# Kernel optimization log

Hardware: AMD Instinct MI355X
Metric: run time of the kernel (lower is better)

Reference implementation:

```python
import jax, jax.numpy as jnp
import numpy as np

EPS = 1e-8  # torch F.cosine_similarity eps


def _cos_attn_masked(x, roi, h):
    """Replicates MultiHeadedAttention_2: per-head cosine similarity, relu,
    global top-k(4) column mask (torch advanced-indexing semantics), roi mask.
    x: (B,num,C), roi: (B,num,num). Returns (B,num,num,h)."""
    B, num, C = x.shape
    dk = C // h
    xh = x.reshape(B, num, h, dk)
    n = jnp.linalg.norm(xh, axis=-1)                       # (B,num,h)
    dots = jnp.einsum('bihd,bjhd->bijh', xh, xh)           # (B,i,j,h)
    denom = jnp.maximum(n[:, :, None, :] * n[:, None, :, :], EPS)
    a = jax.nn.relu(dots / denom)                          # (B,i,j,h)
    # torch: values, idces = topk(attn, 4, dim=2); atten_mask[:, :, idces, :] = 1
    # -> column j is unmasked iff j appears ANYWHERE in idces (global union).
    _, idx = jax.lax.top_k(jnp.moveaxis(a, 2, -1), 4)      # (B,i,h,4) over j
    vec = jnp.zeros((num,), a.dtype).at[idx.reshape(-1)].set(1.0)
    return a * roi[:, :, :, None] * vec[None, None, :, None]


def _gconv_relu(x, w, b):
    """Grouped 1x1 Conv1d + ReLU. x: (B,C,num), w: (g, co_g, ci_g), b: (co,)."""
    B, C, num = x.shape
    g, co_g, ci_g = w.shape
    xg = x.reshape(B, g, ci_g, num)
    y = jnp.einsum('goc,bgcn->bgon', w, xg).reshape(B, g * co_g, num)
    return jax.nn.relu(y + b[None, :, None])


def setup_inputs() -> dict:
    key = jax.random.key(0)
    ks = jax.random.split(key, 10)
    B, num = 4, 1024
    c_in, c_mid, c_out, group = 256, 256, 256, 4
    inp = {
        'input': jax.random.normal(ks[0], (B, num, c_in), jnp.float32),
        'masks_roi': jax.random.randint(ks[1], (B, num, num), 0, 2, jnp.int32),
        'score_mask': jax.random.randint(ks[2], (B, num), 0, 2, jnp.int32),
        'gt_feat': jax.random.normal(ks[3], (B, num, c_in), jnp.float32),
        'w1': jax.random.normal(ks[4], (group, c_mid // group, c_in // group), jnp.float32) * 0.05,
        'b1': jax.random.normal(ks[5], (c_mid,), jnp.float32) * 0.05,
        'w2': jax.random.normal(ks[6], (group, c_out // group, c_mid // group), jnp.float32) * 0.05,
        'b2': jax.random.normal(ks[7], (c_out,), jnp.float32) * 0.05,
        'gt_w': jax.random.normal(ks[8], (c_out, c_in), jnp.float32) * 0.05,
        'gt_b': jax.random.normal(ks[9], (c_out,), jnp.float32) * 0.05,
        # module init explicitly zeroes LayerNorm weight AND bias
        'ln_w': jnp.zeros((c_out,), jnp.float32),
        'ln_b': jnp.zeros((c_out,), jnp.float32),
        'multi_head': 4,
    }
    return inp


def reference(input, masks_roi, score_mask, gt_feat, w1, b1, w2, b2, gt_w, gt_b, ln_w, ln_b, multi_head):
    h = multi_head
    B, num, C = input.shape
    dt = input.dtype
    sm = score_mask.astype(dt)
    roi = masks_roi.astype(dt) * sm[:, None, :]
    f_mask = jax.vmap(jnp.diag)((sm == 0).astype(dt))      # (B,num,num)

    gts = jax.nn.relu(gt_feat @ gt_w.T + gt_b).reshape(B, -1, gt_w.shape[0])

    # --- stage 1 ---
    a1 = (_cos_attn_masked(input, roi, h) + f_mask[:, :, :, None]) / 4.0
    p1 = a1.transpose(0, 3, 2, 1)                          # (B,h,j,i)
    out1 = _gconv_relu(input.transpose(0, 2, 1), w1, b1)   # (B,mid,num)
    mid = out1.shape[1]
    o1m = jnp.einsum('bhcj,bhji->bhci', out1.reshape(B, h, mid // h, num), p1)
    out1 = out1 + o1m.reshape(B, mid, num)

    # --- stage 2 ---
    a2 = (_cos_attn_masked(out1.transpose(0, 2, 1), roi, h) + f_mask[:, :, :, None]) / 4.0
    p2 = a2.transpose(0, 3, 2, 1)
    out2 = _gconv_relu(out1, w2, b2)                       # (B,out,num)
    co = out2.shape[1]
    o2m = jnp.einsum('bhcj,bhji->bhci', out2.reshape(B, h, co // h, num), p2)
    y = o2m.reshape(B, co, num).transpose(0, 2, 1)         # (B,num,out)

    # LayerNorm(eps=1e-6) -- weight/bias zero-initialized per the module
    mu = y.mean(-1, keepdims=True)
    var = y.var(-1, keepdims=True)
    node_feat = (y - mu) / jnp.sqrt(var + 1e-6) * ln_w + ln_b

    out2 = out2 + node_feat.transpose(0, 2, 1)
    return out2.transpose(0, 2, 1), gts, node_feat


if __name__ == '__main__':
    o = reference(**setup_inputs())
    print([x.shape for x in o])
```

## Files before the change

### kernel.cpp

```cpp
#include <hip/hip_runtime.h>
#include <hip/hip_bf16.h>

#define B_    4
#define NUM   1024
#define CH    256
#define HEADS 4
#define DK    64
#define LDK   72
#define NJC   4

typedef __hip_bfloat16 bf;
typedef __attribute__((ext_vector_type(8))) short short8;
typedef __attribute__((ext_vector_type(4))) float f32x4;
typedef unsigned long long u64;
typedef unsigned u32;

#define SEG_ ((size_t)B_ * NUM * CH)

__device__ inline bf tobf(float v) { return __float2bfloat16(v); }

__device__ inline void stage_tile(const float* __restrict__ src, size_t row0,
                                  int col0, int rowstride, bf (*dst)[LDK], int tid) {
  int r = tid >> 4, c4 = (tid & 15) * 4;
  #pragma unroll
  for (int it = 0; it < 4; ++it) {
    int row = r + it * 16;
    const float4 v = *(const float4*)&src[(row0 + row) * (size_t)rowstride + col0 + c4];
    union { bf h4[4]; short4 s4; } u;
    u.h4[0] = tobf(v.x); u.h4[1] = tobf(v.y); u.h4[2] = tobf(v.z); u.h4[3] = tobf(v.w);
    *(short4*)&dst[row][c4] = u.s4;
  }
}

__device__ inline void load_afrag_bf(const bf* __restrict__ arow, int quad, short8 af[2]) {
  af[0] = *(const short8*)&arow[quad * 8];
  af[1] = *(const short8*)&arow[32 + quad * 8];
}

__device__ inline u32 umax(u32 a, u32 b) { return a > b ? a : b; }
__device__ inline u32 umin(u32 a, u32 b) { return a < b ? a : b; }

__device__ inline void sort4(u32& k0, u32& k1, u32& k2, u32& k3) {
  u32 h;
  h = umax(k0, k1); k1 = umin(k0, k1); k0 = h;
  h = umax(k2, k3); k3 = umin(k2, k3); k2 = h;
  h = umax(k0, k2); k2 = umin(k0, k2); k0 = h;
  h = umax(k1, k3); k3 = umin(k1, k3); k1 = h;
  h = umax(k1, k2); k2 = umin(k1, k2); k1 = h;
}

__device__ inline void merge4(u32 t[4], u32 o0, u32 o1, u32 o2, u32 o3) {
  u32 m0 = umax(t[0], o3), m1 = umax(t[1], o2);
  u32 m2 = umax(t[2], o1), m3 = umax(t[3], o0);
  u32 h;
  h = umax(m0, m2); m2 = umin(m0, m2); m0 = h;
  h = umax(m1, m3); m3 = umin(m1, m3); m1 = h;
  h = umax(m0, m1); m1 = umin(m0, m1); m0 = h;
  h = umax(m2, m3); m3 = umin(m2, m3); m2 = h;
  t[0] = m0; t[1] = m1; t[2] = m2; t[3] = m3;
}

__device__ inline void conv_body(
    char* SM, int m0, int g, int tid,
    const float* __restrict__ x, const float* __restrict__ parts,
    const float* __restrict__ w,
    const float* __restrict__ bias, const int* __restrict__ smask,
    float seedbase, float* __restrict__ out, float* __restrict__ out2,
    float* __restrict__ rn, bf* __restrict__ xbf) {
  float (*Xs)[65] = (float(*)[65])SM;
  float (*Wsm)[65] = (float(*)[65])(SM + 16640);
  const int tx = tid & 15, ty = tid >> 4;
  #pragma unroll
  for (int l = 0; l < 16; ++l) {
    int idx = tid + l * 256; int r = idx >> 6, c = idx & 63;
    size_t gi = (size_t)(m0 + r) * CH + g * DK + c;
    float v = x[gi];
    if (parts)
      v += parts[gi] + parts[SEG_ + gi] + parts[2 * SEG_ + gi] + parts[3 * SEG_ + gi];
    Xs[r][c] = v;
    Wsm[r][c] = w[g * DK * DK + r * DK + c];
  }
  __syncthreads();
  {
    int r = tid >> 4, c4 = (tid & 15) * 4;
    #pragma unroll
    for (int it = 0; it < 4; ++it) {
      int row = r + it * 16;
      union { bf h4[4]; short4 s4; } u;
      u.h4[0] = tobf(Xs[row][c4]);     u.h4[1] = tobf(Xs[row][c4 + 1]);
      u.h4[2] = tobf(Xs[row][c4 + 2]); u.h4[3] = tobf(Xs[row][c4 + 3]);
      *(short4*)&xbf[(size_t)(m0 + row) * CH + g * DK + c4] = u.s4;
    }
  }
  {
    int wv = tid >> 6, lane = tid & 63;
    int row = wv * 16 + (lane >> 2), part = lane & 3;
    float s = 0.f;
    #pragma unroll
    for (int k = 0; k < 16; ++k) {
      float v = Xs[row][part * 16 + k];
      s += v * v;
    }
    s += __shfl_xor(s, 1, 64);
    s += __shfl_xor(s, 2, 64);
    if (part == 0)
      rn[(size_t)(m0 + row) * HEADS + g] = 1.0f / fmaxf(sqrtf(s), 1e-4f);
  }
  float acc[4][4] = {};
  #pragma unroll 8
  for (int k = 0; k < DK; ++k) {
    float av[4], bv[4];
    #pragma unroll
    for (int i = 0; i < 4; ++i) av[i] = Xs[ty * 4 + i][k];
    #pragma unroll
    for (int j = 0; j < 4; ++j) bv[j] = Wsm[tx * 4 + j][k];
    #pragma unroll
    for (int i = 0; i < 4; ++i)
      #pragma unroll
      for (int j = 0; j < 4; ++j) acc[i][j] += av[i] * bv[j];
  }
  #pragma unroll
  for (int i = 0; i < 4; ++i) {
    int row = m0 + ty * 4 + i;
    float seed = seedbase + ((smask[row] == 0) ? 0.25f : 0.f);
    #pragma unroll
    for (int j = 0; j < 4; ++j) {
      int o = g * DK + tx * 4 + j;
      size_t idx = (size_t)row * CH + o;
      float v = fmaxf(acc[i][j] + bias[o], 0.f);
      out[idx] = v;
      out2[idx] = v * seed;
    }
  }
}

__device__ inline void gts_body(
    char* SM, int m0, int n0, int tid,
    const float* __restrict__ gf, const float* __restrict__ gw,
    const float* __restrict__ gb, float* __restrict__ out) {
  bf (*As)[LDK] = (bf(*)[LDK])SM;
  bf (*Bs)[LDK] = (bf(*)[LDK])(SM + 9216);
  const int lane = tid & 63, w = tid >> 6;
  const int m = lane & 15, quad = lane >> 4;
  f32x4 acc[4] = {{0.f,0.f,0.f,0.f},{0.f,0.f,0.f,0.f},{0.f,0.f,0.f,0.f},{0.f,0.f,0.f,0.f}};
  for (int k0 = 0; k0 < 256; k0 += 64) {
    __syncthreads();
    stage_tile(gf, m0, k0, 256, As, tid);
    stage_tile(gw, n0, k0, 256, Bs, tid);
    __syncthreads();
    #pragma unroll
    for (int kb = 0; kb < 2; ++kb) {
      short8 a = *(const short8*)&As[w * 16 + m][kb * 32 + quad * 8];
      #pragma unroll
      for (int nt = 0; nt < 4; ++nt) {
        short8 bb = *(const short8*)&Bs[nt * 16 + m][kb * 32 + quad * 8];
        acc[nt] = __builtin_amdgcn_mfma_f32_16x16x32_bf16(a, bb, acc[nt], 0, 0, 0);
      }
    }
  }
  #pragma unroll
  for (int nt = 0; nt < 4; ++nt)
    #pragma unroll
    for (int r = 0; r < 4; ++r) {
      int row = m0 + w * 16 + quad * 4 + r, col = n0 + nt * 16 + m;
      out[(size_t)row * 256 + col] = fmaxf(acc[nt][r] + gb[col], 0.f);
    }
}

__device__ inline void pack_body(int blkrow, int tid, const int* __restrict__ mroi,
                                 const int* __restrict__ smask, u64* __restrict__ pk,
                                 float* __restrict__ v1, float* __restrict__ v2) {
  if (blkrow < 4) {
    int i = blkrow * 256 + tid;
    v1[i] = 0.f; v2[i] = 0.f;
  }
  int row = blkrow * 4 + (tid >> 6);
  int lane = tid & 63;
  int b = row >> 10;
  const int* mr = &mroi[(size_t)row * NUM];
  const int* sm = &smask[b * NUM];
  #pragma unroll
  for (int wd = 0; wd < 16; ++wd) {
    int j = wd * 64 + lane;
    u64 word = __ballot((mr[j] != 0) && (sm[j] != 0));
    if (lane == 0) pk[(size_t)row * 16 + wd] = word;
  }
}

__global__ __launch_bounds__(256) void head_kernel(
    const float* __restrict__ x, const float* __restrict__ w1,
    const float* __restrict__ b1, const int* __restrict__ smask,
    float* __restrict__ X1, float* __restrict__ F1, float* __restrict__ rn,
    bf* __restrict__ xbf,
    const float* __restrict__ gf, const float* __restrict__ gw,
    const float* __restrict__ gb, float* __restrict__ gts_out,
    const int* __restrict__ mroi, u64* __restrict__ pk,
    float* __restrict__ v1, float* __restrict__ v2) {
  __shared__ __align__(16) char SM[33280];
  const int tid = threadIdx.x;
  if (blockIdx.y < 4) {
    conv_body(SM, blockIdx.x * 64, blockIdx.y, tid, x, nullptr, w1, b1, smask,
              1.0f, X1, F1, rn, xbf);
  } else if (blockIdx.y < 8) {
    gts_body(SM, blockIdx.x * 64, (blockIdx.y - 4) * 64, tid, gf, gw, gb, gts_out);
  } else {
    pack_body((blockIdx.y - 8) * 64 + blockIdx.x, tid, mroi, smask, pk, v1, v2);
  }
}

__global__ __launch_bounds__(256) void conv_kernel(
    const float* __restrict__ x, const float* __restrict__ parts,
    const float* __restrict__ w,
    const float* __restrict__ bias, const int* __restrict__ smask,
    float seedbase, float* __restrict__ out, float* __restrict__ out2,
    float* __restrict__ rn, bf* __restrict__ xbf) {
  __shared__ __align__(16) char SM[33280];
  conv_body(SM, blockIdx.x * 64, blockIdx.y, threadIdx.x, x, parts, w, bias, smask,
            seedbase, out, out2, rn, xbf);
}

__global__ __launch_bounds__(256) void score_topk_kernel(
    const bf* __restrict__ xbf, const float* __restrict__ rn,
    const u64* __restrict__ pk, bf* __restrict__ wsout,
    u32* __restrict__ candK) {
  __shared__ __align__(16) bf Xj[2][64][LDK];
  const int b = blockIdx.z, h = blockIdx.y;
  const int it = blockIdx.x >> 2, jc = blockIdx.x & 3;
  const int i0 = it * 64;
  const int tid = threadIdx.x, lane = tid & 63, w = tid >> 6;
  const int m = lane & 15, quad = lane >> 4;
  const int srow = tid >> 3, schunk = tid & 7;

  short8 afrag[2];
  load_afrag_bf(&xbf[((size_t)b * NUM + i0 + w * 16 + m) * CH + h * DK], quad, afrag);

  u32 keys[4][4] = {};

  const int row0 = i0 + w * 16 + quad * 4;
  bf* wp[4];
  const u64* pkp[4];
  #pragma unroll
  for (int r = 0; r < 4; ++r) {
    wp[r]  = wsout + ((size_t)(b * HEADS + h) * NUM + row0 + r) * NUM + jc * 256 + m;
    pkp[r] = pk + ((size_t)b * NUM + row0 + r) * 16 + jc * 4;
  }
  const float* rnp = rn + ((size_t)b * NUM + jc * 256 + m) * HEADS + h;

  auto sload = [&](int jt, short8& n0, short8& n1) {
    size_t base = (size_t)b * NUM + jc * 256 + jt * 64;
    n0 = *(const short8*)&xbf[(base + srow) * CH + h * DK + schunk * 8];
    n1 = *(const short8*)&xbf[(base + srow + 32) * CH + h * DK + schunk * 8];
  };
  auto swrite = [&](int buf, short8 n0, short8 n1) {
    *(short8*)&Xj[buf][srow][schunk * 8] = n0;
    *(short8*)&Xj[buf][srow + 32][schunk * 8] = n1;
  };

  {
    short8 n0, n1;
    sload(0, n0, n1);
    swrite(0, n0, n1);
  }
  __syncthreads();

  #pragma unroll
  for (int jt = 0; jt < 4; ++jt) {
    const int cur = jt & 1;
    short8 n0, n1;
    if (jt < 3) sload(jt + 1, n0, n1);
    u64 wrm[4];
    float rnj4[4];
    #pragma unroll
    for (int r = 0; r < 4; ++r)
      wrm[r] = pkp[r][jt] >> m;
    #pragma unroll
    for (int nt = 0; nt < 4; ++nt)
      rnj4[nt] = rnp[(jt * 64 + nt * 16) * HEADS];

    f32x4 acc[4];
    #pragma unroll
    for (int nt = 0; nt < 4; ++nt) {
      acc[nt] = (f32x4){0.f, 0.f, 0.f, 0.f};
      #pragma unroll
      for (int kb = 0; kb < 2; ++kb) {
        short8 bb = *(const short8*)&Xj[cur][nt * 16 + m][kb * 32 + quad * 8];
        acc[nt] = __builtin_amdgcn_mfma_f32_16x16x32_bf16(afrag[kb], bb, acc[nt], 0, 0, 0);
      }
    }
    const u32 jinv0 = 1023u - (u32)(jc * 256 + jt * 64 + m);
    #pragma unroll
    for (int r = 0; r < 4; ++r) {
      float kv0 = fmaxf(acc[0][r] * rnj4[0], 0.f);
      float kv1 = fmaxf(acc[1][r] * rnj4[1], 0.f);
      float kv2 = fmaxf(acc[2][r] * rnj4[2], 0.f);
      float kv3 = fmaxf(acc[3][r] * rnj4[3], 0.f);
      u32 k0 = (__float_as_uint(kv0) & 0xFFFFFC00u) | jinv0;
      u32 k1 = (__float_as_uint(kv1) & 0xFFFFFC00u) | (jinv0 - 16u);
      u32 k2 = (__float_as_uint(kv2) & 0xFFFFFC00u) | (jinv0 - 32u);
      u32 k3 = (__float_as_uint(kv3) & 0xFFFFFC00u) | (jinv0 - 48u);
      sort4(k0, k1, k2, k3);
      merge4(keys[r], k0, k1, k2, k3);
      wp[r][jt * 64 +  0] = tobf((wrm[r] &        1ull) ? kv0 : 0.f);
      wp[r][jt * 64 + 16] = tobf((wrm[r] >> 16 &  1ull) ? kv1 : 0.f);
      wp[r][jt * 64 + 32] = tobf((wrm[r] >> 32 &  1ull) ? kv2 : 0.f);
      wp[r][jt * 64 + 48] = tobf((wrm[r] >> 48 &  1ull) ? kv3 : 0.f);
    }
    if (jt < 3) swrite(cur ^ 1, n0, n1);
    __syncthreads();
  }

  #pragma unroll
  for (int st = 1; st < 16; st <<= 1) {
    #pragma unroll
    for (int r = 0; r < 4; ++r) {
      u32 o0 = (u32)__shfl_xor((int)keys[r][0], st, 64);
      u32 o1 = (u32)__shfl_xor((int)keys[r][1], st, 64);
      u32 o2 = (u32)__shfl_xor((int)keys[r][2], st, 64);
      u32 o3 = (u32)__shfl_xor((int)keys[r][3], st, 64);
      merge4(keys[r], o0, o1, o2, o3);
    }
  }
  if (m == 0) {
    #pragma unroll
    for (int r = 0; r < 4; ++r) {
      int rl = w * 16 + quad * 4 + r;
      u32* dst = &candK[(size_t)((((b * HEADS + h) * 16 + it) * NJC + jc) * 64 + rl) * 4];
      #pragma unroll
      for (int q = 0; q < 4; ++q) dst[q] = keys[r][q];
    }
  }
}

__global__ __launch_bounds__(256) void topk_merge_kernel(
    const u32* __restrict__ candK, float* __restrict__ vec) {
  int t = blockIdx.x * 256 + threadIdx.x;
  int bhit = t >> 6, rl = t & 63;
  u32 best[4] = {};
  #pragma unroll
  for (int jc = 0; jc < NJC; ++jc) {
    const u32* c = &candK[(size_t)((bhit * NJC + jc) * 64 + rl) * 4];
    merge4(best, c[0], c[1], c[2], c[3]);
  }
  #pragma unroll
  for (int q = 0; q < 4; ++q)
    vec[1023u - (best[q] & 0x3FFu)] = 1.0f;
}

__global__ __launch_bounds__(256) void pv_kernel(
    const bf* __restrict__ wsin, const float* __restrict__ conv,
    const float* __restrict__ rn, const float* __restrict__ vec,
    float* __restrict__ outp) {
  __shared__ __align__(16) bf Cv[2][64][LDK];
  const int b = blockIdx.z, h = blockIdx.y;
  const int it = blockIdx.x >> 2, jc = blockIdx.x & 3;
  const int i0 = it * 64, jbase = jc * 256;
  const int tid = threadIdx.x, lane = tid & 63, w = tid >> 6;
  const int m = lane & 15, quad = lane >> 4;
  const int jr = tid >> 4, c4 = tid & 15;

  float rni4[4];
  #pragma unroll
  for (int r = 0; r < 4; ++r)
    rni4[r] = 0.25f * rn[((size_t)b * NUM + i0 + w * 16 + quad * 4 + r) * HEADS + h];

  const size_t wsrow = ((size_t)(b * HEADS + h) * NUM + i0 + w * 16 + m) * NUM + jbase;

  f32x4 om[4] = {{0.f,0.f,0.f,0.f},{0.f,0.f,0.f,0.f},{0.f,0.f,0.f,0.f},{0.f,0.f,0.f,0.f}};

  float4 pre[4]; float psc[4];
  auto issue = [&](int jt) {
    #pragma unroll
    for (int itt = 0; itt < 4; ++itt) {
      int j = jbase + jt * 64 + jr + itt * 16;
      psc[itt] = vec[j];
      pre[itt] = *(const float4*)&conv[((size_t)b * NUM + j) * CH + h * DK + c4 * 4];
    }
  };
  auto lwrite = [&](int buf) {
    #pragma unroll
    for (int itt = 0; itt < 4; ++itt) {
      int j = jr + itt * 16;
      Cv[buf][c4 * 4 + 0][j] = tobf(pre[itt].x * psc[itt]);
      Cv[buf][c4 * 4 + 1][j] = tobf(pre[itt].y * psc[itt]);
      Cv[buf][c4 * 4 + 2][j] = tobf(pre[itt].z * psc[itt]);
      Cv[buf][c4 * 4 + 3][j] = tobf(pre[itt].w * psc[itt]);
    }
  };

  issue(0); lwrite(0);
  short8 a0 = *(const short8*)&wsin[wsrow + quad * 8];
  short8 a1 = *(const short8*)&wsin[wsrow + 32 + quad * 8];

  for (int jt = 0; jt < 4; ++jt) {
    const int cur = jt & 1;
    short8 na0, na1;
    if (jt < 3) {
      issue(jt + 1);
      na0 = *(const short8*)&wsin[wsrow + (jt + 1) * 64 + quad * 8];
      na1 = *(const short8*)&wsin[wsrow + (jt + 1) * 64 + 32 + quad * 8];
    }
    __syncthreads();
    #pragma unroll
    for (int ct = 0; ct < 4; ++ct)
      om[ct] = __builtin_amdgcn_mfma_f32_16x16x32_bf16(
          a0, *(const short8*)&Cv[cur][ct * 16 + m][quad * 8], om[ct], 0, 0, 0);
    #pragma unroll
    for (int ct = 0; ct < 4; ++ct)
      om[ct] = __builtin_amdgcn_mfma_f32_16x16x32_bf16(
          a1, *(const short8*)&Cv[cur][ct * 16 + m][32 + quad * 8], om[ct], 0, 0, 0);
    if (jt < 3) { lwrite(cur ^ 1); a0 = na0; a1 = na1; }
  }

  const size_t ob = (size_t)(jc * B_ + b) * NUM;
  #pragma unroll
  for (int ct = 0; ct < 4; ++ct)
    #pragma unroll
    for (int r = 0; r < 4; ++r) {
      size_t idx = (ob + i0 + w * 16 + quad * 4 + r) * CH + h * DK + ct * 16 + m;
      outp[idx] = om[ct][r] * rni4[r];
    }
}

__global__ __launch_bounds__(256) void final_kernel(
    float* __restrict__ ybnf, float* __restrict__ out0,
    const float* __restrict__ lnw, const float* __restrict__ lnb,
    const float* __restrict__ parts) {
  __shared__ float r1[4];
  __shared__ float r2[4];
  int bn = blockIdx.x;
  int c = threadIdx.x;
  size_t idx = (size_t)bn * CH + c;
  float y = ybnf[idx] + parts[idx] + parts[SEG_ + idx]
          + parts[2 * SEG_ + idx] + parts[3 * SEG_ + idx];
  float x2v = out0[idx];
  float s = y;
  #pragma unroll
  for (int off = 32; off; off >>= 1) s += __shfl_down(s, off, 64);
  int wave = c >> 6, lane = c & 63;
  if (lane == 0) r1[wave] = s;
  __syncthreads();
  float mu = (r1[0] + r1[1] + r1[2] + r1[3]) * (1.f / 256.f);
  float d = y - mu;
  float s2 = d * d;
  #pragma unroll
  for (int off = 32; off; off >>= 1) s2 += __shfl_down(s2, off, 64);
  if (lane == 0) r2[wave] = s2;
  __syncthreads();
  float var = (r2[0] + r2[1] + r2[2] + r2[3]) * (1.f / 256.f);
  float nf = d * rsqrtf(var + 1e-6f) * lnw[c] + lnb[c];
  ybnf[idx] = nf;
  out0[idx] = x2v + nf;
}

extern "C" void kernel_launch(void* const* d_in, const int* in_sizes, int n_in,
                              void* d_out, int out_size, void* d_ws, size_t ws_size,
                              hipStream_t stream) {
  const float* input = (const float*)d_in[0];
  const int* mroi = (const int*)d_in[1];
  const int* smask = (const int*)d_in[2];
  const float* gt_feat = (const float*)d_in[3];
  const float* w1 = (const float*)d_in[4];
  const float* b1 = (const float*)d_in[5];
  const float* w2 = (const float*)d_in[6];
  const float* b2 = (const float*)d_in[7];
  const float* gt_w = (const float*)d_in[8];
  const float* gt_b = (const float*)d_in[9];
  const float* lnw = (const float*)d_in[10];
  const float* lnb = (const float*)d_in[11];

  const size_t SEG = SEG_;
  float* out0 = (float*)d_out;
  float* gts = out0 + SEG;
  float* nfreg = out0 + 2 * SEG;

  float* F1 = (float*)d_ws;
  float* RN = F1 + SEG;
  float* VEC1 = RN + (size_t)B_ * NUM * HEADS;
  float* VEC2 = VEC1 + NUM;
  u64* PK = (u64*)(VEC2 + NUM);
  bf* XBF = (bf*)(PK + (size_t)B_ * NUM * 16);
  bf* WSC = XBF + SEG;
  float* P = (float*)(WSC + (size_t)B_ * HEADS * NUM * NUM);
  u32* candK = (u32*)P;

  float* X1 = nfreg;
  float* X2 = out0;
  float* Yb = nfreg;

  head_kernel<<<dim3(64, 24), 256, 0, stream>>>(
      input, w1, b1, smask, X1, F1, RN, XBF,
      gt_feat, gt_w, gt_b, gts, mroi, PK, VEC1, VEC2);

  score_topk_kernel<<<dim3(16 * NJC, HEADS, B_), 256, 0, stream>>>(
      XBF, RN, PK, WSC, candK);
  topk_merge_kernel<<<64, 256, 0, stream>>>(candK, VEC1);
  pv_kernel<<<dim3(16 * NJC, HEADS, B_), 256, 0, stream>>>(WSC, X1, RN, VEC1, P);

  conv_kernel<<<dim3(64, 4), 256, 0, stream>>>(F1, P, w2, b2, smask, 0.0f, X2, Yb, RN, XBF);
  score_topk_kernel<<<dim3(16 * NJC, HEADS, B_), 256, 0, stream>>>(
      XBF, RN, PK, WSC, candK);
  topk_merge_kernel<<<64, 256, 0, stream>>>(candK, VEC2);
  pv_kernel<<<dim3(16 * NJC, HEADS, B_), 256, 0, stream>>>(WSC, X2, RN, VEC2, P);

  final_kernel<<<4096, 256, 0, stream>>>(Yb, X2, lnw, lnb, P);
}
```

Measured before the change: 199.4 us.

## Split score_topk j-tiles across two wave groups with 512-thread blocks

The score/top-k kernel now runs 512 threads per block. Two groups of four waves each handle half of the four j-tiles, so each wave does two tiles instead of four. All four Xj tiles are staged into shared memory once up front, which removes the per-tile double-buffer syncs. The two groups' partial top-4 keys are merged through a small shared exchange buffer. This adds parallelism and latency hiding per block, at the cost of more LDS per block and an extra barrier and merge step.

```diff
diff --git a/kernel.cpp b/kernel.cpp
--- a/kernel.cpp
+++ b/kernel.cpp
@@ -219,60 +219,53 @@
             seedbase, out, out2, rn, xbf);
 }
 
-__global__ __launch_bounds__(256) void score_topk_kernel(
+__global__ __launch_bounds__(512, 6) void score_topk_kernel(
     const bf* __restrict__ xbf, const float* __restrict__ rn,
     const u64* __restrict__ pk, bf* __restrict__ wsout,
     u32* __restrict__ candK) {
-  __shared__ __align__(16) bf Xj[2][64][LDK];
+  __shared__ __align__(16) bf Xj[4][64][LDK];
+  __shared__ u32 cexch[64][4];
   const int b = blockIdx.z, h = blockIdx.y;
   const int it = blockIdx.x >> 2, jc = blockIdx.x & 3;
   const int i0 = it * 64;
-  const int tid = threadIdx.x, lane = tid & 63, w = tid >> 6;
+  const int tid = threadIdx.x, lane = tid & 63, wv = tid >> 6;
   const int m = lane & 15, quad = lane >> 4;
+  const int g2 = wv >> 2, rw = wv & 3;
   const int srow = tid >> 3, schunk = tid & 7;
 
+  {
+    short8 st0, st1, st2, st3;
+    const bf* sb = &xbf[((size_t)b * NUM + jc * 256 + srow) * CH + h * DK + schunk * 8];
+    st0 = *(const short8*)&sb[0 * 64 * CH];
+    st1 = *(const short8*)&sb[1 * 64 * CH];
+    st2 = *(const short8*)&sb[2 * 64 * CH];
+    st3 = *(const short8*)&sb[3 * 64 * CH];
+    *(short8*)&Xj[0][srow][schunk * 8] = st0;
+    *(short8*)&Xj[1][srow][schunk * 8] = st1;
+    *(short8*)&Xj[2][srow][schunk * 8] = st2;
+    *(short8*)&Xj[3][srow][schunk * 8] = st3;
+  }
+
   short8 afrag[2];
-  load_afrag_bf(&xbf[((size_t)b * NUM + i0 + w * 16 + m) * CH + h * DK], quad, afrag);
+  load_afrag_bf(&xbf[((size_t)b * NUM + i0 + rw * 16 + m) * CH + h * DK], quad, afrag);
 
   u32 keys[4][4] = {};
 
-  const int row0 = i0 + w * 16 + quad * 4;
-  bf* wp[4];
-  const u64* pkp[4];
-  #pragma unroll
-  for (int r = 0; r < 4; ++r) {
-    wp[r]  = wsout + ((size_t)(b * HEADS + h) * NUM + row0 + r) * NUM + jc * 256 + m;
-    pkp[r] = pk + ((size_t)b * NUM + row0 + r) * 16 + jc * 4;
-  }
+  const int row0 = i0 + rw * 16 + quad * 4;
+  bf* wpb = wsout + ((size_t)(b * HEADS + h) * NUM + row0) * NUM + jc * 256 + m;
+  const u64* pkb = pk + ((size_t)b * NUM + row0) * 16 + jc * 4;
   const float* rnp = rn + ((size_t)b * NUM + jc * 256 + m) * HEADS + h;
 
-  auto sload = [&](int jt, short8& n0, short8& n1) {
-    size_t base = (size_t)b * NUM + jc * 256 + jt * 64;
-    n0 = *(const short8*)&xbf[(base + srow) * CH + h * DK + schunk * 8];
-    n1 = *(const short8*)&xbf[(base + srow + 32) * CH + h * DK + schunk * 8];
-  };
-  auto swrite = [&](int buf, short8 n0, short8 n1) {
-    *(short8*)&Xj[buf][srow][schunk * 8] = n0;
-    *(short8*)&Xj[buf][srow + 32][schunk * 8] = n1;
-  };
-
-  {
-    short8 n0, n1;
-    sload(0, n0, n1);
-    swrite(0, n0, n1);
-  }
   __syncthreads();
 
   #pragma unroll
-  for (int jt = 0; jt < 4; ++jt) {
-    const int cur = jt & 1;
-    short8 n0, n1;
-    if (jt < 3) sload(jt + 1, n0, n1);
+  for (int tt = 0; tt < 2; ++tt) {
+    const int jt = g2 * 2 + tt;
     u64 wrm[4];
     float rnj4[4];
     #pragma unroll
     for (int r = 0; r < 4; ++r)
-      wrm[r] = pkp[r][jt] >> m;
+      wrm[r] = pkb[r * 16 + jt] >> m;
     #pragma unroll
     for (int nt = 0; nt < 4; ++nt)
       rnj4[nt] = rnp[(jt * 64 + nt * 16) * HEADS];
@@ -283,7 +276,7 @@
       acc[nt] = (f32x4){0.f, 0.f, 0.f, 0.f};
       #pragma unroll
       for (int kb = 0; kb < 2; ++kb) {
-        short8 bb = *(const short8*)&Xj[cur][nt * 16 + m][kb * 32 + quad * 8];
+        short8 bb = *(const short8*)&Xj[jt][nt * 16 + m][kb * 32 + quad * 8];
         acc[nt] = __builtin_amdgcn_mfma_f32_16x16x32_bf16(afrag[kb], bb, acc[nt], 0, 0, 0);
       }
     }
@@ -300,13 +293,18 @@
       u32 k3 = (__float_as_uint(kv3) & 0xFFFFFC00u) | (jinv0 - 48u);
       sort4(k0, k1, k2, k3);
       merge4(keys[r], k0, k1, k2, k3);
-      wp[r][jt * 64 +  0] = tobf((wrm[r] &        1ull) ? kv0 : 0.f);
-      wp[r][jt * 64 + 16] = tobf((wrm[r] >> 16 &  1ull) ? kv1 : 0.f);
-      wp[r][jt * 64 + 32] = tobf((wrm[r] >> 32 &  1ull) ? kv2 : 0.f);
-      wp[r][jt * 64 + 48] = tobf((wrm[r] >> 48 &  1ull) ? kv3 : 0.f);
-    }
-    if (jt < 3) swrite(cur ^ 1, n0, n1);
-    __syncthreads();
+      if (tt == 0) {
+        wpb[r * NUM + g2 * 128 +  0] = tobf((wrm[r] &       1ull) ? kv0 : 0.f);
+        wpb[r * NUM + g2 * 128 + 16] = tobf((wrm[r] >> 16 & 1ull) ? kv1 : 0.f);
+        wpb[r * NUM + g2 * 128 + 32] = tobf((wrm[r] >> 32 & 1ull) ? kv2 : 0.f);
+        wpb[r * NUM + g2 * 128 + 48] = tobf((wrm[r] >> 48 & 1ull) ? kv3 : 0.f);
+      } else {
+        wpb[r * NUM + g2 * 128 + 64 +  0] = tobf((wrm[r] &       1ull) ? kv0 : 0.f);
+        wpb[r * NUM + g2 * 128 + 64 + 16] = tobf((wrm[r] >> 16 & 1ull) ? kv1 : 0.f);
+        wpb[r * NUM + g2 * 128 + 64 + 32] = tobf((wrm[r] >> 32 & 1ull) ? kv2 : 0.f);
+        wpb[r * NUM + g2 * 128 + 64 + 48] = tobf((wrm[r] >> 48 & 1ull) ? kv3 : 0.f);
+      }
+    }
   }
 
   #pragma unroll
@@ -320,10 +318,20 @@
       merge4(keys[r], o0, o1, o2, o3);
     }
   }
-  if (m == 0) {
+  if (g2 == 1 && m == 0) {
     #pragma unroll
     for (int r = 0; r < 4; ++r) {
-      int rl = w * 16 + quad * 4 + r;
+      int rl = rw * 16 + quad * 4 + r;
+      #pragma unroll
+      for (int q = 0; q < 4; ++q) cexch[rl][q] = keys[r][q];
+    }
+  }
+  __syncthreads();
+  if (g2 == 0 && m == 0) {
+    #pragma unroll
+    for (int r = 0; r < 4; ++r) {
+      int rl = rw * 16 + quad * 4 + r;
+      merge4(keys[r], cexch[rl][0], cexch[rl][1], cexch[rl][2], cexch[rl][3]);
       u32* dst = &candK[(size_t)((((b * HEADS + h) * 16 + it) * NJC + jc) * 64 + rl) * 4];
       #pragma unroll
       for (int q = 0; q < 4; ++q) dst[q] = keys[r][q];
@@ -491,13 +499,13 @@
       input, w1, b1, smask, X1, F1, RN, XBF,
       gt_feat, gt_w, gt_b, gts, mroi, PK, VEC1, VEC2);
 
-  score_topk_kernel<<<dim3(16 * NJC, HEADS, B_), 256, 0, stream>>>(
+  score_topk_kernel<<<dim3(16 * NJC, HEADS, B_), 512, 0, stream>>>(
       XBF, RN, PK, WSC, candK);
   topk_merge_kernel<<<64, 256, 0, stream>>>(candK, VEC1);
   pv_kernel<<<dim3(16 * NJC, HEADS, B_), 256, 0, stream>>>(WSC, X1, RN, VEC1, P);
 
   conv_kernel<<<dim3(64, 4), 256, 0, stream>>>(F1, P, w2, b2, smask, 0.0f, X2, Yb, RN, XBF);
-  score_topk_kernel<<<dim3(16 * NJC, HEADS, B_), 256, 0, stream>>>(
+  score_topk_kernel<<<dim3(16 * NJC, HEADS, B_), 512, 0, stream>>>(
       XBF, RN, PK, WSC, candK);
   topk_merge_kernel<<<64, 256, 0, stream>>>(candK, VEC2);
   pv_kernel<<<dim3(16 * NJC, HEADS, B_), 256, 0, stream>>>(WSC, X2, RN, VEC2, P);
```

After: 197.4 us. Within noise of the previous version (-1.0%).

## Fuse top-k merge into score kernel using 1024-thread blocks and LDS exchange

Applied to the files above, without the earlier changes.

The score/top-k kernel now runs one 1024-thread block per (b,h,row-tile), with four wave groups each covering a 256-column chunk. Partial top-4 candidates are merged through shared memory and written straight into the column mask. This removes the separate topk_merge launch and the global candidate round-trip, twice per forward. In exchange the grid shrinks from 1024 to 256 blocks, shared memory per block grows, and the launch-bounds hint of 4 blocks per SM may not be reachable, which could reduce occupancy.

```diff
diff --git a/kernel.cpp b/kernel.cpp
--- a/kernel.cpp
+++ b/kernel.cpp
@@ -219,41 +219,29 @@
             seedbase, out, out2, rn, xbf);
 }
 
-__global__ __launch_bounds__(256) void score_topk_kernel(
+__global__ __launch_bounds__(1024, 4) void score_topk_kernel(
     const bf* __restrict__ xbf, const float* __restrict__ rn,
     const u64* __restrict__ pk, bf* __restrict__ wsout,
-    u32* __restrict__ candK) {
-  __shared__ __align__(16) bf Xj[2][64][LDK];
-  const int b = blockIdx.z, h = blockIdx.y;
-  const int it = blockIdx.x >> 2, jc = blockIdx.x & 3;
+    float* __restrict__ vec) {
+  __shared__ __align__(16) bf Xj[2][4][64][LDK];
+  __shared__ u32 cexch[3][64][4];
+  const int b = blockIdx.z, h = blockIdx.y, it = blockIdx.x;
   const int i0 = it * 64;
-  const int tid = threadIdx.x, lane = tid & 63, w = tid >> 6;
+  const int tid = threadIdx.x, lane = tid & 63, wv = tid >> 6;
   const int m = lane & 15, quad = lane >> 4;
-  const int srow = tid >> 3, schunk = tid & 7;
-
-  short8 afrag[2];
-  load_afrag_bf(&xbf[((size_t)b * NUM + i0 + w * 16 + m) * CH + h * DK], quad, afrag);
-
-  u32 keys[4][4] = {};
-
-  const int row0 = i0 + w * 16 + quad * 4;
-  bf* wp[4];
-  const u64* pkp[4];
-  #pragma unroll
-  for (int r = 0; r < 4; ++r) {
-    wp[r]  = wsout + ((size_t)(b * HEADS + h) * NUM + row0 + r) * NUM + jc * 256 + m;
-    pkp[r] = pk + ((size_t)b * NUM + row0 + r) * 16 + jc * 4;
-  }
-  const float* rnp = rn + ((size_t)b * NUM + jc * 256 + m) * HEADS + h;
-
-  auto sload = [&](int jt, short8& n0, short8& n1) {
-    size_t base = (size_t)b * NUM + jc * 256 + jt * 64;
-    n0 = *(const short8*)&xbf[(base + srow) * CH + h * DK + schunk * 8];
-    n1 = *(const short8*)&xbf[(base + srow + 32) * CH + h * DK + schunk * 8];
+  const int g4 = wv >> 2, rw = wv & 3;
+  const int slot = tid & 511, srow = slot >> 3, schunk = slot & 7;
+  const int tpair = tid >> 9;
+
+  auto sload = [&](int k, short8& n0, short8& n1) {
+    size_t base = (size_t)b * NUM;
+    int t0 = (tpair * 2 + 0) * 4 + k, t1 = (tpair * 2 + 1) * 4 + k;
+    n0 = *(const short8*)&xbf[(base + t0 * 64 + srow) * CH + h * DK + schunk * 8];
+    n1 = *(const short8*)&xbf[(base + t1 * 64 + srow) * CH + h * DK + schunk * 8];
   };
   auto swrite = [&](int buf, short8 n0, short8 n1) {
-    *(short8*)&Xj[buf][srow][schunk * 8] = n0;
-    *(short8*)&Xj[buf][srow + 32][schunk * 8] = n1;
+    *(short8*)&Xj[buf][tpair * 2 + 0][srow][schunk * 8] = n0;
+    *(short8*)&Xj[buf][tpair * 2 + 1][srow][schunk * 8] = n1;
   };
 
   {
@@ -261,21 +249,34 @@
     sload(0, n0, n1);
     swrite(0, n0, n1);
   }
+
+  short8 afrag[2];
+  load_afrag_bf(&xbf[((size_t)b * NUM + i0 + rw * 16 + m) * CH + h * DK], quad, afrag);
+
+  u32 keys[4][4] = {};
+
+  const int row0 = i0 + rw * 16 + quad * 4;
+  bf* wpb = wsout + ((size_t)(b * HEADS + h) * NUM + row0) * NUM + m;
+  const u64* pkb = pk + ((size_t)b * NUM + row0) * 16;
+  const float* rnp = rn + ((size_t)b * NUM + m) * HEADS + h;
+
   __syncthreads();
 
   #pragma unroll
-  for (int jt = 0; jt < 4; ++jt) {
-    const int cur = jt & 1;
+  for (int k = 0; k < 4; ++k) {
+    const int cur = k & 1;
+    const int jt = g4 * 4 + k;
+    const int j0 = jt * 64;
     short8 n0, n1;
-    if (jt < 3) sload(jt + 1, n0, n1);
+    if (k < 3) sload(k + 1, n0, n1);
     u64 wrm[4];
     float rnj4[4];
     #pragma unroll
     for (int r = 0; r < 4; ++r)
-      wrm[r] = pkp[r][jt] >> m;
+      wrm[r] = pkb[r * 16 + jt] >> m;
     #pragma unroll
     for (int nt = 0; nt < 4; ++nt)
-      rnj4[nt] = rnp[(jt * 64 + nt * 16) * HEADS];
+      rnj4[nt] = rnp[(j0 + nt * 16) * HEADS];
 
     f32x4 acc[4];
     #pragma unroll
@@ -283,11 +284,11 @@
       acc[nt] = (f32x4){0.f, 0.f, 0.f, 0.f};
       #pragma unroll
       for (int kb = 0; kb < 2; ++kb) {
-        short8 bb = *(const short8*)&Xj[cur][nt * 16 + m][kb * 32 + quad * 8];
+        short8 bb = *(const short8*)&Xj[cur][g4][nt * 16 + m][kb * 32 + quad * 8];
         acc[nt] = __builtin_amdgcn_mfma_f32_16x16x32_bf16(afrag[kb], bb, acc[nt], 0, 0, 0);
       }
     }
-    const u32 jinv0 = 1023u - (u32)(jc * 256 + jt * 64 + m);
+    const u32 jinv0 = 1023u - (u32)(j0 + m);
     #pragma unroll
     for (int r = 0; r < 4; ++r) {
       float kv0 = fmaxf(acc[0][r] * rnj4[0], 0.f);
@@ -300,12 +301,12 @@
       u32 k3 = (__float_as_uint(kv3) & 0xFFFFFC00u) | (jinv0 - 48u);
       sort4(k0, k1, k2, k3);
       merge4(keys[r], k0, k1, k2, k3);
-      wp[r][jt * 64 +  0] = tobf((wrm[r] &        1ull) ? kv0 : 0.f);
-      wp[r][jt * 64 + 16] = tobf((wrm[r] >> 16 &  1ull) ? kv1 : 0.f);
-      wp[r][jt * 64 + 32] = tobf((wrm[r] >> 32 &  1ull) ? kv2 : 0.f);
-      wp[r][jt * 64 + 48] = tobf((wrm[r] >> 48 &  1ull) ? kv3 : 0.f);
-    }
-    if (jt < 3) swrite(cur ^ 1, n0, n1);
+      wpb[r * NUM + j0 +  0] = tobf((wrm[r] &        1ull) ? kv0 : 0.f);
+      wpb[r * NUM + j0 + 16] = tobf((wrm[r] >> 16 &  1ull) ? kv1 : 0.f);
+      wpb[r * NUM + j0 + 32] = tobf((wrm[r] >> 32 &  1ull) ? kv2 : 0.f);
+      wpb[r * NUM + j0 + 48] = tobf((wrm[r] >> 48 &  1ull) ? kv3 : 0.f);
+    }
+    if (k < 3) swrite(cur ^ 1, n0, n1);
     __syncthreads();
   }
 
@@ -320,30 +321,27 @@
       merge4(keys[r], o0, o1, o2, o3);
     }
   }
-  if (m == 0) {
+  if (g4 != 0 && m == 0) {
     #pragma unroll
     for (int r = 0; r < 4; ++r) {
-      int rl = w * 16 + quad * 4 + r;
-      u32* dst = &candK[(size_t)((((b * HEADS + h) * 16 + it) * NJC + jc) * 64 + rl) * 4];
+      int rl = rw * 16 + quad * 4 + r;
       #pragma unroll
-      for (int q = 0; q < 4; ++q) dst[q] = keys[r][q];
-    }
-  }
-}
-
-__global__ __launch_bounds__(256) void topk_merge_kernel(
-    const u32* __restrict__ candK, float* __restrict__ vec) {
-  int t = blockIdx.x * 256 + threadIdx.x;
-  int bhit = t >> 6, rl = t & 63;
-  u32 best[4] = {};
-  #pragma unroll
-  for (int jc = 0; jc < NJC; ++jc) {
-    const u32* c = &candK[(size_t)((bhit * NJC + jc) * 64 + rl) * 4];
-    merge4(best, c[0], c[1], c[2], c[3]);
-  }
-  #pragma unroll
-  for (int q = 0; q < 4; ++q)
-    vec[1023u - (best[q] & 0x3FFu)] = 1.0f;
+      for (int q = 0; q < 4; ++q) cexch[g4 - 1][rl][q] = keys[r][q];
+    }
+  }
+  __syncthreads();
+  if (g4 == 0 && m == 0) {
+    #pragma unroll
+    for (int r = 0; r < 4; ++r) {
+      int rl = rw * 16 + quad * 4 + r;
+      merge4(keys[r], cexch[0][rl][0], cexch[0][rl][1], cexch[0][rl][2], cexch[0][rl][3]);
+      merge4(keys[r], cexch[1][rl][0], cexch[1][rl][1], cexch[1][rl][2], cexch[1][rl][3]);
+      merge4(keys[r], cexch[2][rl][0], cexch[2][rl][1], cexch[2][rl][2], cexch[2][rl][3]);
+      #pragma unroll
+      for (int q = 0; q < 4; ++q)
+        vec[1023u - (keys[r][q] & 0x3FFu)] = 1.0f;
+    }
+  }
 }
 
 __global__ __launch_bounds__(256) void pv_kernel(
@@ -481,7 +479,6 @@
   bf* XBF = (bf*)(PK + (size_t)B_ * NUM * 16);
   bf* WSC = XBF + SEG;
   float* P = (float*)(WSC + (size_t)B_ * HEADS * NUM * NUM);
-  u32* candK = (u32*)P;
 
   float* X1 = nfreg;
   float* X2 = out0;
@@ -491,15 +488,13 @@
       input, w1, b1, smask, X1, F1, RN, XBF,
       gt_feat, gt_w, gt_b, gts, mroi, PK, VEC1, VEC2);
 
-  score_topk_kernel<<<dim3(16 * NJC, HEADS, B_), 256, 0, stream>>>(
-      XBF, RN, PK, WSC, candK);
-  topk_merge_kernel<<<64, 256, 0, stream>>>(candK, VEC1);
+  score_topk_kernel<<<dim3(16, HEADS, B_), 1024, 0, stream>>>(
+      XBF, RN, PK, WSC, VEC1);
   pv_kernel<<<dim3(16 * NJC, HEADS, B_), 256, 0, stream>>>(WSC, X1, RN, VEC1, P);
 
   conv_kernel<<<dim3(64, 4), 256, 0, stream>>>(F1, P, w2, b2, smask, 0.0f, X2, Yb, RN, XBF);
-  score_topk_kernel<<<dim3(16 * NJC, HEADS, B_), 256, 0, stream>>>(
-      XBF, RN, PK, WSC, candK);
-  topk_merge_kernel<<<64, 256, 0, stream>>>(candK, VEC2);
+  score_topk_kernel<<<dim3(16, HEADS, B_), 1024, 0, stream>>>(
+      XBF, RN, PK, WSC, VEC2);
   pv_kernel<<<dim3(16 * NJC, HEADS, B_), 256, 0, stream>>>(WSC, X2, RN, VEC2, P);
 
   final_kernel<<<4096, 256, 0, stream>>>(Yb, X2, lnw, lnb, P);
```

Result: no change. 197.7 us (-0.9%).
